# Kernel optimization log

Measured on AMD Instinct MI355X. Metric: run time of the kernel, lower is better.

The kernel has to match this reference:

```python
import jax, jax.numpy as jnp
import numpy as np

EPS = 0.0  # module eps default
N, C = 524288, 128


def setup_inputs() -> dict:
    key = jax.random.key(0)
    x = jax.random.normal(key, (N, C), dtype=jnp.float32)
    return {"x": x}


def reference(x):
    n, c = x.shape
    # mean over batch (H=W=1 in the original NCHW view)
    m = jnp.mean(x, axis=0, keepdims=True)          # [1, C]
    xn = x - m                                      # [N, C]
    # covariance: T @ T.T / (N-1) with T = xn.T -> [C, C]
    f_cov = jnp.einsum('ni,nj->ij', xn, xn) / (n - 1)
    eye = jnp.eye(c, dtype=x.dtype)
    f_cov_shrinked = (1.0 - EPS) * f_cov + EPS * eye
    L = jnp.linalg.cholesky(f_cov_shrinked)         # lower-triangular
    # inv_sqrt = L^{-1} via triangular solve of L @ X = I
    inv_sqrt = jax.scipy.linalg.solve_triangular(L, eye, lower=True)  # [C, C]
    # 1x1 conv with kernel inv_sqrt[o, i] == xn @ inv_sqrt.T
    decorrelated = xn @ inv_sqrt.T                  # [N, C]
    return decorrelated
```

## Files before the change

### kernel.cpp

```cpp
#include <hip/hip_runtime.h>

#define NROWS 524288
#define NCH 128
#define GSTR 40

typedef __attribute__((ext_vector_type(8))) short bf16x8;
typedef __attribute__((ext_vector_type(4))) float f32x4;

static __device__ __forceinline__ unsigned short f2bf_rne(float f) {
    unsigned u = __float_as_uint(f);
    return (unsigned short)((u + 0x7FFFu + ((u >> 16) & 1u)) >> 16);
}

static __device__ __forceinline__ bf16x8 ldfrag(const unsigned short* base, int c, int s0) {
    int m = (c >> 3) & 12;
    return *(const bf16x8*)(base + c * GSTR + 2 * (s0 ^ m));
}

#define PACKW1(B, c, x0, x1, csacc) do {                                      \
    unsigned u0 = __float_as_uint(x0), u1 = __float_as_uint(x1);              \
    unsigned packH = (u0 >> 16) | (u1 & 0xFFFF0000u);                         \
    float l0_ = 2.0f * ((x0) - __uint_as_float(u0 & 0xFFFF0000u));            \
    float l1_ = 2.0f * ((x1) - __uint_as_float(u1 & 0xFFFF0000u));            \
    unsigned packL = (unsigned)f2bf_rne(l0_) | ((unsigned)f2bf_rne(l1_) << 16); \
    int idx_ = (c) * GSTR + 2 * (p ^ (cg & 12));                              \
    *(unsigned*)&XT[B][0][idx_] = packH;                                      \
    *(unsigned*)&XT[B][1][idx_] = packL;                                      \
    csacc += (x0) + (x1);                                                     \
} while (0)

#define LOADR(ci, r0, r1, r2, r3) do {                                        \
    const float4* s4_ = (const float4*)x + ((size_t)(ci) * 32 + 2 * p) * 32 + cg * 2; \
    r0 = s4_[0]; r1 = s4_[1]; r2 = s4_[32]; r3 = s4_[33];                     \
} while (0)

#define PACKALL(B, r0, r1, r2, r3) do {                                       \
    PACKW1(B, cg * 8 + 0, r0.x, r2.x, cs0);                                   \
    PACKW1(B, cg * 8 + 1, r0.y, r2.y, cs1);                                   \
    PACKW1(B, cg * 8 + 2, r0.z, r2.z, cs2);                                   \
    PACKW1(B, cg * 8 + 3, r0.w, r2.w, cs3);                                   \
    PACKW1(B, cg * 8 + 4, r1.x, r3.x, cs4);                                   \
    PACKW1(B, cg * 8 + 5, r1.y, r3.y, cs5);                                   \
    PACKW1(B, cg * 8 + 6, r1.z, r3.z, cs6);                                   \
    PACKW1(B, cg * 8 + 7, r1.w, r3.w, cs7);                                   \
} while (0)

#define MFMA_STEP(B) do {                                                     \
    const unsigned short* Xh = &XT[B][0][0];                                  \
    const unsigned short* Xl = &XT[B][1][0];                                  \
    bf16x8 ah0 = ldfrag(Xh, (2 * w + 0) * 16 + lc, ls);                       \
    bf16x8 ah1 = ldfrag(Xh, (2 * w + 1) * 16 + lc, ls);                       \
    _Pragma("unroll")                                                         \
    for (int tj = 0; tj < 8; ++tj) {                                          \
        bf16x8 bh = ldfrag(Xh, tj * 16 + lc, ls);                             \
        bf16x8 bl = ldfrag(Xl, tj * 16 + lc, ls);                             \
        acc[0][tj] = __builtin_amdgcn_mfma_f32_16x16x32_bf16(ah0, bh, acc[0][tj], 0, 0, 0); \
        acc[0][tj] = __builtin_amdgcn_mfma_f32_16x16x32_bf16(ah0, bl, acc[0][tj], 0, 0, 0); \
        acc[1][tj] = __builtin_amdgcn_mfma_f32_16x16x32_bf16(ah1, bh, acc[1][tj], 0, 0, 0); \
        acc[1][tj] = __builtin_amdgcn_mfma_f32_16x16x32_bf16(ah1, bl, acc[1][tj], 0, 0, 0); \
    }                                                                         \
} while (0)

template <int STORE>
__global__ __launch_bounds__(256, 3) void k_gram(const float* __restrict__ x,
                                                 float* __restrict__ part,
                                                 float* __restrict__ colpart,
                                                 float* __restrict__ gram,
                                                 float* __restrict__ colsum,
                                                 int cpb) {
    __shared__ __align__(16) unsigned short XT[2][2][128 * GSTR];
    const int tid = threadIdx.x;
    const int w = tid >> 6;
    const int l = tid & 63;
    const int lc = l & 15;
    const int ls = (l >> 4) * 4;
    const int p = tid >> 4;
    const int cg = tid & 15;

    f32x4 acc[2][8];
#pragma unroll
    for (int a = 0; a < 2; ++a)
#pragma unroll
        for (int t = 0; t < 8; ++t) acc[a][t] = (f32x4){0.f, 0.f, 0.f, 0.f};
    float cs0 = 0.f, cs1 = 0.f, cs2 = 0.f, cs3 = 0.f;
    float cs4 = 0.f, cs5 = 0.f, cs6 = 0.f, cs7 = 0.f;

    const int c0 = blockIdx.x * cpb;
    float4 a0, a1, a2, a3, b0, b1, b2, b3;

    LOADR(c0 + 0, a0, a1, a2, a3);
    LOADR(c0 + 1, b0, b1, b2, b3);
    PACKALL(0, a0, a1, a2, a3);
    __syncthreads();

#pragma unroll 1
    for (int t = 0; t < cpb; t += 2) {
        MFMA_STEP(0);
        PACKALL(1, b0, b1, b2, b3);
        if (t + 2 < cpb) LOADR(c0 + t + 2, a0, a1, a2, a3);
        __syncthreads();
        MFMA_STEP(1);
        if (t + 2 < cpb) {
            PACKALL(0, a0, a1, a2, a3);
            if (t + 3 < cpb) LOADR(c0 + t + 3, b0, b1, b2, b3);
            __syncthreads();
        }
    }

    __syncthreads();
    float* cls = (float*)&XT[0][0][0];
    cls[(cg * 8 + 0) * 16 + p] = cs0;
    cls[(cg * 8 + 1) * 16 + p] = cs1;
    cls[(cg * 8 + 2) * 16 + p] = cs2;
    cls[(cg * 8 + 3) * 16 + p] = cs3;
    cls[(cg * 8 + 4) * 16 + p] = cs4;
    cls[(cg * 8 + 5) * 16 + p] = cs5;
    cls[(cg * 8 + 6) * 16 + p] = cs6;
    cls[(cg * 8 + 7) * 16 + p] = cs7;
    __syncthreads();
    float csr = 0.f;
    if (tid < 128) {
#pragma unroll
        for (int pp = 0; pp < 16; ++pp) csr += cls[tid * 16 + pp];
    }

    if (STORE) {
        float* pb = part + (size_t)blockIdx.x * 16384;
#pragma unroll
        for (int a = 0; a < 2; ++a)
#pragma unroll
            for (int tj = 0; tj < 8; ++tj)
#pragma unroll
                for (int q = 0; q < 4; ++q) {
                    int row = (2 * w + a) * 16 + (l >> 4) * 4 + q;
                    int col = tj * 16 + lc;
                    pb[row * NCH + col] = acc[a][tj][q];
                }
        if (tid < 128) colpart[blockIdx.x * 128 + tid] = csr;
    } else {
#pragma unroll
        for (int a = 0; a < 2; ++a)
#pragma unroll
            for (int tj = 0; tj < 8; ++tj)
#pragma unroll
                for (int q = 0; q < 4; ++q) {
                    int row = (2 * w + a) * 16 + (l >> 4) * 4 + q;
                    int col = tj * 16 + lc;
                    atomicAdd(&gram[row * NCH + col], acc[a][tj][q]);
                }
        if (tid < 128) atomicAdd(&colsum[tid], csr);
    }
}

__global__ __launch_bounds__(256) void k_reduce1(const float* __restrict__ part,
                                                 const float* __restrict__ colpart,
                                                 float* __restrict__ part2,
                                                 float* __restrict__ col2,
                                                 int NG) {
    const int b = blockIdx.x;
    if (b < 16 * NG) {
        const int g = b >> 4;
        const int sl = b & 15;
        const int e4 = sl * 1024 + threadIdx.x * 4;
        const float* p0 = part + (size_t)g * 32 * 16384 + e4;
        float4 s = {0.f, 0.f, 0.f, 0.f};
#pragma unroll
        for (int k = 0; k < 32; ++k) {
            float4 v = *(const float4*)(p0 + (size_t)k * 16384);
            s.x += v.x; s.y += v.y; s.z += v.z; s.w += v.w;
        }
        *(float4*)(part2 + (size_t)g * 16384 + e4) = s;
    } else {
        const int g = b - 16 * NG;
        if (threadIdx.x < 128) {
            const float* c0 = colpart + g * 32 * 128 + threadIdx.x;
            float s = 0.f;
#pragma unroll
            for (int k = 0; k < 32; ++k) s += c0[k * 128];
            col2[g * 128 + threadIdx.x] = s;
        }
    }
}

__global__ __launch_bounds__(256) void k_reduce2(const float* __restrict__ part2,
                                                 const float* __restrict__ col2,
                                                 float* __restrict__ gram,
                                                 float* __restrict__ colsum,
                                                 int NG) {
    const int b = blockIdx.x;
    if (b < 16) {
        const int e4 = b * 1024 + threadIdx.x * 4;
        float4 s = {0.f, 0.f, 0.f, 0.f};
#pragma unroll 8
        for (int g = 0; g < NG; ++g) {
            float4 v = *(const float4*)(part2 + (size_t)g * 16384 + e4);
            s.x += v.x; s.y += v.y; s.z += v.z; s.w += v.w;
        }
        *(float4*)(gram + e4) = s;
    } else if (threadIdx.x < 128) {
        float s = 0.f;
#pragma unroll 8
        for (int g = 0; g < NG; ++g) s += col2[g * 128 + threadIdx.x];
        colsum[threadIdx.x] = s;
    }
}

__global__ __launch_bounds__(1024) void k_chol(const float* __restrict__ gram,
                                               const float* __restrict__ colsum,
                                               float* __restrict__ Wout,
                                               float* __restrict__ mout) {
    __shared__ float C[128][264];
    __shared__ __align__(16) float Praw[4][264];
    __shared__ float m[128];
    __shared__ float dsq[128];
    const int tid = threadIdx.x;
    const int rs = tid >> 5;
    const int cs = tid & 31;

    if (tid < 128) {
        m[tid] = colsum[tid] * (1.0f / (float)NROWS);
        mout[tid] = m[tid];
    }
    __syncthreads();
    for (int idx = tid; idx < 128 * 128; idx += 1024) {
        int i = idx >> 7, j = idx & 127;
        float g = 0.5f * (gram[i * NCH + j] + gram[j * NCH + i]);
        C[i][128 + j] = (g - (float)NROWS * m[i] * m[j]) * (1.0f / (float)(NROWS - 1));
        C[i][j] = (i == j) ? 1.0f : 0.0f;
    }
    __syncthreads();

#pragma unroll 1
    for (int kb = 0; kb < 128; kb += 4) {
        if (tid < 264) {
            int r = tid / 66, g = tid % 66;
            *(float4*)&Praw[r][g * 4] = *(const float4*)&C[kb + r][g * 4];
        }
        __syncthreads();

        float M00 = C[kb + 0][128 + kb + 0], M01 = C[kb + 0][128 + kb + 1];
        float M02 = C[kb + 0][128 + kb + 2], M03 = C[kb + 0][128 + kb + 3];
        float M10 = C[kb + 1][128 + kb + 0], M11 = C[kb + 1][128 + kb + 1];
        float M12 = C[kb + 1][128 + kb + 2], M13 = C[kb + 1][128 + kb + 3];
        float M20 = C[kb + 2][128 + kb + 0], M21 = C[kb + 2][128 + kb + 1];
        float M22 = C[kb + 2][128 + kb + 2], M23 = C[kb + 2][128 + kb + 3];
        float M30 = C[kb + 3][128 + kb + 0], M31 = C[kb + 3][128 + kb + 1];
        float M32 = C[kb + 3][128 + kb + 2], M33 = C[kb + 3][128 + kb + 3];

        float rd0 = 1.0f / M00;
        float g10 = M10 * rd0, g20 = M20 * rd0, g30 = M30 * rd0;
        float N11 = M11 - g10 * M01, N12 = M12 - g10 * M02, N13 = M13 - g10 * M03;
        float N21 = M21 - g20 * M01, N22 = M22 - g20 * M02, N23 = M23 - g20 * M03;
        float N31 = M31 - g30 * M01, N32 = M32 - g30 * M02, N33 = M33 - g30 * M03;
        float rd1 = 1.0f / N11;
        float g21 = N21 * rd1, g31 = N31 * rd1;
        float P22 = N22 - g21 * N12, P23 = N23 - g21 * N13;
        float P32 = N32 - g31 * N12, P33 = N33 - g31 * N13;
        float rd2 = 1.0f / P22;
        float g32 = P32 * rd2;
        float Q33 = P33 - g32 * P23;
        float rd3 = 1.0f / Q33;

        float T10 = -g10;
        float T20 = -g20 - g21 * T10, T21 = -g21;
        float T30 = -g30 - g31 * T10 - g32 * T20;
        float T31 = -g31 - g32 * T21;
        float T32 = -g32;

        if (tid == 0) {
            dsq[kb + 0] = 1.0f / sqrtf(M00);
            dsq[kb + 1] = 1.0f / sqrtf(N11);
            dsq[kb + 2] = 1.0f / sqrtf(P22);
            dsq[kb + 3] = 1.0f / sqrtf(Q33);
        }

        const bool doB = (cs <= (kb >> 2));
        const int gRel = (kb >> 2) + 1 + cs;
        const bool doA = (gRel < 32);

        float4 Pb0, Pb1, Pb2, Pb3, Pa0, Pa1, Pa2, Pa3;
        if (doB) {
            Pb0 = *(const float4*)&Praw[0][cs * 4];
            Pb1 = *(const float4*)&Praw[1][cs * 4];
            Pb2 = *(const float4*)&Praw[2][cs * 4];
            Pb3 = *(const float4*)&Praw[3][cs * 4];
        }
        if (doA) {
            Pa0 = *(const float4*)&Praw[0][128 + gRel * 4];
            Pa1 = *(const float4*)&Praw[1][128 + gRel * 4];
            Pa2 = *(const float4*)&Praw[2][128 + gRel * 4];
            Pa3 = *(const float4*)&Praw[3][128 + gRel * 4];
        }

        for (int j = kb + 1 + rs; j < 128; j += 32) {
            const int tmax = j - kb;
            float a0 = C[j][128 + kb + 0], a1 = C[j][128 + kb + 1];
            float a2 = C[j][128 + kb + 2], a3 = C[j][128 + kb + 3];
            float f0 = a0 * rd0;
            float c0 = f0, c1 = 0.f, c2 = 0.f, c3 = 0.f;
            if (tmax > 1) {
                float f1 = (a1 - c0 * M01) * rd1;
                c0 += f1 * T10; c1 = f1;
                if (tmax > 2) {
                    float f2 = (a2 - c0 * M02 - c1 * M12) * rd2;
                    c0 += f2 * T20; c1 += f2 * T21; c2 = f2;
                    if (tmax > 3) {
                        float f3 = (a3 - c0 * M03 - c1 * M13 - c2 * M23) * rd3;
                        c0 += f3 * T30; c1 += f3 * T31; c2 += f3 * T32; c3 = f3;
                    }
                }
            }
            if (doB) {
                float4 v = *(const float4*)&C[j][cs * 4];
                v.x -= c0 * Pb0.x + c1 * Pb1.x + c2 * Pb2.x + c3 * Pb3.x;
                v.y -= c0 * Pb0.y + c1 * Pb1.y + c2 * Pb2.y + c3 * Pb3.y;
                v.z -= c0 * Pb0.z + c1 * Pb1.z + c2 * Pb2.z + c3 * Pb3.z;
                v.w -= c0 * Pb0.w + c1 * Pb1.w + c2 * Pb2.w + c3 * Pb3.w;
                *(float4*)&C[j][cs * 4] = v;
            }
            if (doA) {
                float4 v = *(const float4*)&C[j][128 + gRel * 4];
                v.x -= c0 * Pa0.x + c1 * Pa1.x + c2 * Pa2.x + c3 * Pa3.x;
                v.y -= c0 * Pa0.y + c1 * Pa1.y + c2 * Pa2.y + c3 * Pa3.y;
                v.z -= c0 * Pa0.z + c1 * Pa1.z + c2 * Pa2.z + c3 * Pa3.z;
                v.w -= c0 * Pa0.w + c1 * Pa1.w + c2 * Pa2.w + c3 * Pa3.w;
                *(float4*)&C[j][128 + gRel * 4] = v;
            }
        }
        __syncthreads();
    }

    for (int idx = tid; idx < 128 * 128; idx += 1024) {
        int j = idx >> 7, c = idx & 127;
        float vv = (c < j) ? C[j][c] * dsq[j] : ((c == j) ? dsq[j] : 0.0f);
        Wout[idx] = vv;
    }
}

__global__ __launch_bounds__(256, 3) void k_apply(const float* __restrict__ x,
                                                  const float* __restrict__ Wg,
                                                  const float* __restrict__ mg,
                                                  float* __restrict__ out) {
    __shared__ __align__(16) unsigned char XS[128 * 128];
    __shared__ float msh[128];
    const int tid = threadIdx.x;
    const int w = tid >> 6, l = tid & 63;
    const int lc = l & 15, la = l >> 4;

    if (tid < 32) *(float4*)&msh[tid * 4] = *(const float4*)&mg[tid * 4];
    __syncthreads();

    bf16x8 rfrag[2][4];
#pragma unroll
    for (int tjl = 0; tjl < 2; ++tjl) {
        int j = (w * 2 + tjl) * 16 + lc;
#pragma unroll
        for (int ks = 0; ks < 4; ++ks) {
            int i0 = ks * 32 + la * 8;
            float4 wa = *(const float4*)&Wg[j * 128 + i0];
            float4 wb = *(const float4*)&Wg[j * 128 + i0 + 4];
            rfrag[tjl][ks][0] = f2bf_rne(wa.x - ((j == i0 + 0) ? 1.0f : 0.0f));
            rfrag[tjl][ks][1] = f2bf_rne(wa.y - ((j == i0 + 1) ? 1.0f : 0.0f));
            rfrag[tjl][ks][2] = f2bf_rne(wa.z - ((j == i0 + 2) ? 1.0f : 0.0f));
            rfrag[tjl][ks][3] = f2bf_rne(wa.w - ((j == i0 + 3) ? 1.0f : 0.0f));
            rfrag[tjl][ks][4] = f2bf_rne(wb.x - ((j == i0 + 4) ? 1.0f : 0.0f));
            rfrag[tjl][ks][5] = f2bf_rne(wb.y - ((j == i0 + 5) ? 1.0f : 0.0f));
            rfrag[tjl][ks][6] = f2bf_rne(wb.z - ((j == i0 + 6) ? 1.0f : 0.0f));
            rfrag[tjl][ks][7] = f2bf_rne(wb.w - ((j == i0 + 7) ? 1.0f : 0.0f));
        }
    }

    f32x4 acc[8][2];
#pragma unroll
    for (int ti = 0; ti < 8; ++ti)
#pragma unroll
        for (int tjl = 0; tjl < 2; ++tjl) acc[ti][tjl] = (f32x4){0.f, 0.f, 0.f, 0.f};

    const size_t rowbase = (size_t)blockIdx.x * 128;

#pragma unroll
    for (int c = 0; c < 2; ++c) {
        const int kb = c * 64;
#pragma unroll
        for (int rep = 0; rep < 8; ++rep) {
            int f = tid + 256 * rep;
            int r = f >> 4, i4 = f & 15;
            float4 vx = *(const float4*)&x[(rowbase + r) * 128 + kb + i4 * 4];
            float4 mv = *(const float4*)&msh[kb + i4 * 4];
            unsigned b0 = f2bf_rne(vx.x - mv.x);
            unsigned b1 = f2bf_rne(vx.y - mv.y);
            unsigned b2 = f2bf_rne(vx.z - mv.z);
            unsigned b3 = f2bf_rne(vx.w - mv.w);
            unsigned off = r * 128 + ((((i4 >> 1) ^ (r & 7))) << 4) + (i4 & 1) * 8;
            *(uint2*)(XS + off) = make_uint2(b0 | (b1 << 16), b2 | (b3 << 16));
        }
        __syncthreads();
#pragma unroll
        for (int ksl = 0; ksl < 2; ++ksl) {
#pragma unroll
            for (int ti = 0; ti < 8; ++ti) {
                int r = ti * 16 + lc;
                int g = ksl * 4 + la;
                bf16x8 af = *(const bf16x8*)(XS + r * 128 + ((g ^ (r & 7)) << 4));
                acc[ti][0] = __builtin_amdgcn_mfma_f32_16x16x32_bf16(af, rfrag[0][c * 2 + ksl], acc[ti][0], 0, 0, 0);
                acc[ti][1] = __builtin_amdgcn_mfma_f32_16x16x32_bf16(af, rfrag[1][c * 2 + ksl], acc[ti][1], 0, 0, 0);
            }
        }
        __syncthreads();
    }

#pragma unroll
    for (int ti = 0; ti < 8; ++ti)
#pragma unroll
        for (int tjl = 0; tjl < 2; ++tjl)
#pragma unroll
            for (int q = 0; q < 4; ++q) {
                int rloc = ti * 16 + la * 4 + q;
                int cglob = (w * 2 + tjl) * 16 + lc;
                size_t a = (rowbase + rloc) * 128 + cglob;
                out[a] = (x[a] - msh[cglob]) + acc[ti][tjl][q];
            }
}

extern "C" void kernel_launch(void* const* d_in, const int* in_sizes, int n_in,
                              void* d_out, int out_size, void* d_ws, size_t ws_size,
                              hipStream_t stream) {
    const float* x = (const float*)d_in[0];
    float* ws = (float*)d_ws;
    float* gram = ws;
    float* colsum = ws + 16384;
    float* W = ws + 16512;
    float* m = ws + 32896;
    float* colpart = ws + 40960;
    float* part = ws + 172032;
    float* out = (float*)d_out;

    int nP = 0;
    for (int cand = 1024; cand >= 256; cand >>= 1) {
        int ng = cand / 32;
        size_t need = ((size_t)172032 + (size_t)cand * 16384 +
                       (size_t)ng * 16384 + (size_t)ng * 128) * sizeof(float);
        if (ws_size >= need) { nP = cand; break; }
    }

    if (nP > 0) {
        const int NG = nP / 32;
        float* part2 = part + (size_t)nP * 16384;
        float* col2 = part2 + (size_t)NG * 16384;
        int cpb = 16384 / nP;
        k_gram<1><<<nP, 256, 0, stream>>>(x, part, colpart, gram, colsum, cpb);
        k_reduce1<<<16 * NG + NG, 256, 0, stream>>>(part, colpart, part2, col2, NG);
        k_reduce2<<<17, 256, 0, stream>>>(part2, col2, gram, colsum, NG);
    } else {
        hipMemsetAsync(d_ws, 0, (16384 + 128) * sizeof(float), stream);
        k_gram<0><<<512, 256, 0, stream>>>(x, part, colpart, gram, colsum, 32);
    }
    k_chol<<<1, 1024, 0, stream>>>(gram, colsum, W, m);
    k_apply<<<NROWS / 128, 256, 0, stream>>>(x, W, m, out);
}
```

Before: 304.4 us.

## Double-buffer Cholesky pivot rows and use lighter barriers in gram kernel

Result: no change. 307.3 us (+0.9%).

```diff
diff --git a/kernel.cpp b/kernel.cpp
--- a/kernel.cpp
+++ b/kernel.cpp
@@ -6,6 +6,8 @@
 
 typedef __attribute__((ext_vector_type(8))) short bf16x8;
 typedef __attribute__((ext_vector_type(4))) float f32x4;
+
+#define BARRIER_ND() asm volatile("s_waitcnt lgkmcnt(0)\ns_barrier" ::: "memory")
 
 static __device__ __forceinline__ unsigned short f2bf_rne(float f) {
     unsigned u = __float_as_uint(f);
@@ -91,19 +93,19 @@
     LOADR(c0 + 0, a0, a1, a2, a3);
     LOADR(c0 + 1, b0, b1, b2, b3);
     PACKALL(0, a0, a1, a2, a3);
-    __syncthreads();
+    BARRIER_ND();
 
 #pragma unroll 1
     for (int t = 0; t < cpb; t += 2) {
         MFMA_STEP(0);
         PACKALL(1, b0, b1, b2, b3);
         if (t + 2 < cpb) LOADR(c0 + t + 2, a0, a1, a2, a3);
-        __syncthreads();
+        BARRIER_ND();
         MFMA_STEP(1);
         if (t + 2 < cpb) {
             PACKALL(0, a0, a1, a2, a3);
             if (t + 3 < cpb) LOADR(c0 + t + 3, b0, b1, b2, b3);
-            __syncthreads();
+            BARRIER_ND();
         }
     }
 
@@ -210,7 +212,7 @@
                                                float* __restrict__ Wout,
                                                float* __restrict__ mout) {
     __shared__ float C[128][264];
-    __shared__ __align__(16) float Praw[4][264];
+    __shared__ __align__(16) float Praw[2][4][264];
     __shared__ float m[128];
     __shared__ float dsq[128];
     const int tid = threadIdx.x;
@@ -229,23 +231,24 @@
         C[i][j] = (i == j) ? 1.0f : 0.0f;
     }
     __syncthreads();
+    if (tid < 264) {
+        int r = tid / 66, g = tid % 66;
+        *(float4*)&Praw[0][r][g * 4] = *(const float4*)&C[r][g * 4];
+    }
+    __syncthreads();
 
 #pragma unroll 1
     for (int kb = 0; kb < 128; kb += 4) {
-        if (tid < 264) {
-            int r = tid / 66, g = tid % 66;
-            *(float4*)&Praw[r][g * 4] = *(const float4*)&C[kb + r][g * 4];
-        }
-        __syncthreads();
-
-        float M00 = C[kb + 0][128 + kb + 0], M01 = C[kb + 0][128 + kb + 1];
-        float M02 = C[kb + 0][128 + kb + 2], M03 = C[kb + 0][128 + kb + 3];
-        float M10 = C[kb + 1][128 + kb + 0], M11 = C[kb + 1][128 + kb + 1];
-        float M12 = C[kb + 1][128 + kb + 2], M13 = C[kb + 1][128 + kb + 3];
-        float M20 = C[kb + 2][128 + kb + 0], M21 = C[kb + 2][128 + kb + 1];
-        float M22 = C[kb + 2][128 + kb + 2], M23 = C[kb + 2][128 + kb + 3];
-        float M30 = C[kb + 3][128 + kb + 0], M31 = C[kb + 3][128 + kb + 1];
-        float M32 = C[kb + 3][128 + kb + 2], M33 = C[kb + 3][128 + kb + 3];
+        const int buf = (kb >> 2) & 1;
+        const float* P0 = Praw[buf][0];
+        const float* P1 = Praw[buf][1];
+        const float* P2 = Praw[buf][2];
+        const float* P3 = Praw[buf][3];
+
+        float M00 = P0[128 + kb + 0], M01 = P0[128 + kb + 1], M02 = P0[128 + kb + 2], M03 = P0[128 + kb + 3];
+        float M10 = P1[128 + kb + 0], M11 = P1[128 + kb + 1], M12 = P1[128 + kb + 2], M13 = P1[128 + kb + 3];
+        float M20 = P2[128 + kb + 0], M21 = P2[128 + kb + 1], M22 = P2[128 + kb + 2], M23 = P2[128 + kb + 3];
+        float M30 = P3[128 + kb + 0], M31 = P3[128 + kb + 1], M32 = P3[128 + kb + 2], M33 = P3[128 + kb + 3];
 
         float rd0 = 1.0f / M00;
         float g10 = M10 * rd0, g20 = M20 * rd0, g30 = M30 * rd0;
@@ -274,22 +277,23 @@
             dsq[kb + 3] = 1.0f / sqrtf(Q33);
         }
 
-        const bool doB = (cs <= (kb >> 2));
-        const int gRel = (kb >> 2) + 1 + cs;
+        const int gs = kb >> 2;
+        const bool doB = (cs <= gs);
+        const int gRel = gs + 1 + cs;
         const bool doA = (gRel < 32);
 
         float4 Pb0, Pb1, Pb2, Pb3, Pa0, Pa1, Pa2, Pa3;
         if (doB) {
-            Pb0 = *(const float4*)&Praw[0][cs * 4];
-            Pb1 = *(const float4*)&Praw[1][cs * 4];
-            Pb2 = *(const float4*)&Praw[2][cs * 4];
-            Pb3 = *(const float4*)&Praw[3][cs * 4];
+            Pb0 = *(const float4*)&P0[cs * 4];
+            Pb1 = *(const float4*)&P1[cs * 4];
+            Pb2 = *(const float4*)&P2[cs * 4];
+            Pb3 = *(const float4*)&P3[cs * 4];
         }
         if (doA) {
-            Pa0 = *(const float4*)&Praw[0][128 + gRel * 4];
-            Pa1 = *(const float4*)&Praw[1][128 + gRel * 4];
-            Pa2 = *(const float4*)&Praw[2][128 + gRel * 4];
-            Pa3 = *(const float4*)&Praw[3][128 + gRel * 4];
+            Pa0 = *(const float4*)&P0[128 + gRel * 4];
+            Pa1 = *(const float4*)&P1[128 + gRel * 4];
+            Pa2 = *(const float4*)&P2[128 + gRel * 4];
+            Pa3 = *(const float4*)&P3[128 + gRel * 4];
         }
 
         for (int j = kb + 1 + rs; j < 128; j += 32) {
@@ -310,6 +314,7 @@
                     }
                 }
             }
+            const bool stage = (j >= kb + 4) && (j < kb + 8);
             if (doB) {
                 float4 v = *(const float4*)&C[j][cs * 4];
                 v.x -= c0 * Pb0.x + c1 * Pb1.x + c2 * Pb2.x + c3 * Pb3.x;
@@ -317,6 +322,7 @@
                 v.z -= c0 * Pb0.z + c1 * Pb1.z + c2 * Pb2.z + c3 * Pb3.z;
                 v.w -= c0 * Pb0.w + c1 * Pb1.w + c2 * Pb2.w + c3 * Pb3.w;
                 *(float4*)&C[j][cs * 4] = v;
+                if (stage) *(float4*)&Praw[buf ^ 1][j - kb - 4][cs * 4] = v;
             }
             if (doA) {
                 float4 v = *(const float4*)&C[j][128 + gRel * 4];
@@ -325,7 +331,13 @@
                 v.z -= c0 * Pa0.z + c1 * Pa1.z + c2 * Pa2.z + c3 * Pa3.z;
                 v.w -= c0 * Pa0.w + c1 * Pa1.w + c2 * Pa2.w + c3 * Pa3.w;
                 *(float4*)&C[j][128 + gRel * 4] = v;
+                if (stage) *(float4*)&Praw[buf ^ 1][j - kb - 4][128 + gRel * 4] = v;
             }
+        }
+        if (tid < 4 && kb + 4 < 128) {
+            float4 e = {0.f, 0.f, 0.f, 0.f};
+            ((float*)&e)[tid] = 1.0f;
+            *(float4*)&Praw[buf ^ 1][tid][(gs + 1) * 4] = e;
         }
         __syncthreads();
     }
```
